# Kernel tuning notes

Measured on AMD Instinct MI355X. Metric: run time of the kernel, lower is better.

The kernel has to match this reference:

```python
import jax, jax.numpy as jnp
import numpy as np

UNITS = 1024
D_MODEL = 1024
H = 16
DK = 64
DV = 64
M = 128
B = 4
S = 1024


def setup_inputs() -> dict:
    key = jax.random.key(0)
    ks = jax.random.split(key, 12)
    s = 1.0 / np.sqrt(D_MODEL)
    inp = {
        "queries": jax.random.normal(ks[0], (B, S, D_MODEL), jnp.float32),
        "keys": jax.random.normal(ks[1], (B, S, D_MODEL), jnp.float32),
        "values": jax.random.normal(ks[2], (B, S, D_MODEL), jnp.float32),
        "Wq": jax.random.normal(ks[3], (D_MODEL, H * DK), jnp.float32) * s,
        "bq": jnp.zeros((H * DK,), jnp.float32),
        "Wk": jax.random.normal(ks[4], (D_MODEL, H * DK), jnp.float32) * s,
        "bk": jnp.zeros((H * DK,), jnp.float32),
        "Wv": jax.random.normal(ks[5], (D_MODEL, H * DV), jnp.float32) * s,
        "bv": jnp.zeros((H * DV,), jnp.float32),
        "Wo": jax.random.normal(ks[6], (H * DV, UNITS), jnp.float32) * (1.0 / np.sqrt(H * DV)),
        "bo": jnp.zeros((UNITS,), jnp.float32),
        "mk": jax.random.normal(ks[7], (1, M, H * DK), jnp.float32) * 0.1,
        "mv": jax.random.normal(ks[8], (1, M, H * DV), jnp.float32) * 0.1,
        "h": H,
    }
    return inp


def reference(queries, keys, values, Wq, bq, Wk, bk, Wv, bv, Wo, bo, mk, mv, h):
    Bq, Sq, _ = queries.shape
    m = mk.shape[1]
    dk = Wk.shape[1] // h
    dv = Wv.shape[1] // h
    scale_m = jnp.sqrt(jnp.asarray(m, queries.dtype))

    # Q projection: [B, h, Sq, dk]
    q = (queries @ Wq + bq).reshape(Bq, Sq, h, dk).transpose(0, 2, 1, 3)

    # K/V projections with m learned memory slots concatenated on the seq axis
    k_flat = jnp.concatenate(
        [keys @ Wk + bk, scale_m * jnp.broadcast_to(mk, (Bq, m, h * dk))], axis=1
    )  # [B, Sk+m, h*dk]
    v_flat = jnp.concatenate(
        [values @ Wv + bv, scale_m * jnp.broadcast_to(mv, (Bq, m, h * dv))], axis=1
    )  # [B, Sk+m, h*dv]
    Skm = k_flat.shape[1]
    k = k_flat.reshape(Bq, Skm, h, dk).transpose(0, 2, 1, 3)  # [B, h, Sk+m, dk]
    v = v_flat.reshape(Bq, Skm, h, dv).transpose(0, 2, 1, 3)  # [B, h, Sk+m, dv]

    # Scaled dot-product attention over sequence + memory slots
    scores = jnp.einsum("bhqd,bhkd->bhqk", q, k) / jnp.sqrt(jnp.asarray(dk, q.dtype))
    attn = jax.nn.softmax(scores, axis=-1)  # [B, h, Sq, Sk+m]
    out = jnp.einsum("bhqk,bhkd->bhqd", attn, v)  # [B, h, Sq, dv]
    out = out.transpose(0, 2, 1, 3).reshape(Bq, Sq, h * dv)
    return out @ Wo + bo
```

## Files before the change

### kernel.cpp

```cpp
#include <hip/hip_runtime.h>

typedef __attribute__((ext_vector_type(8))) __bf16 bf16x8;
typedef __attribute__((ext_vector_type(4))) float f32x4;

#define DEVINL __device__ __forceinline__

constexpr int BZ = 4;
constexpr int SEQ = 1024;
constexpr int DMODEL = 1024;
constexpr int NH = 16;
constexpr int HD = 64;
constexpr int MSLOT = 128;
constexpr int NT = BZ * SEQ;
constexpr int SKM = SEQ + MSLOT;
constexpr int VT_LD = BZ * SKM;
constexpr float SCALE_M = 11.313708498984761f;
constexpr float SCEXP = 0.18033688011112042f;
constexpr size_t OF_QIN  = 0;
constexpr size_t OF_KIN  = OF_QIN  + (size_t)NT * DMODEL;
constexpr size_t OF_VIN  = OF_KIN  + (size_t)NT * DMODEL;
constexpr size_t OF_WQT  = OF_VIN  + (size_t)NT * DMODEL;
constexpr size_t OF_WKT  = OF_WQT  + (size_t)DMODEL * DMODEL;
constexpr size_t OF_WVT  = OF_WKT  + (size_t)DMODEL * DMODEL;
constexpr size_t OF_WOT  = OF_WVT  + (size_t)DMODEL * DMODEL;
constexpr size_t OF_QB   = OF_WOT  + (size_t)DMODEL * DMODEL;
constexpr size_t OF_KPR  = OF_QB   + (size_t)NT * DMODEL;
constexpr size_t OF_KMEM = OF_KPR  + (size_t)NT * DMODEL;
constexpr size_t OF_VTG  = OF_KMEM + (size_t)MSLOT * DMODEL;
constexpr size_t OF_AOUT = OF_VTG  + (size_t)DMODEL * VT_LD;

DEVINL unsigned short f2bf(float f) {
  union { float f; unsigned u; } v; v.f = f;
  unsigned r = v.u + 0x7FFF + ((v.u >> 16) & 1);
  return (unsigned short)(r >> 16);
}

#if __has_builtin(__builtin_amdgcn_cvt_pk_bf16_f32)
DEVINL unsigned pack2(float a, float b) {
  auto t = __builtin_amdgcn_cvt_pk_bf16_f32(a, b);
  unsigned r; __builtin_memcpy(&r, &t, 4); return r;
}
#else
DEVINL unsigned pack2(float a, float b) {
  return (unsigned)f2bf(a) | ((unsigned)f2bf(b) << 16);
}
#endif

#if __has_builtin(__builtin_amdgcn_exp2f)
DEVINL float fast_exp2(float x) { return __builtin_amdgcn_exp2f(x); }
#else
DEVINL float fast_exp2(float x) { return exp2f(x); }
#endif

DEVINL f32x4 mfma16(bf16x8 a, bf16x8 b, f32x4 c) {
  return __builtin_amdgcn_mfma_f32_16x16x32_bf16(a, b, c, 0, 0, 0);
}

DEVINL void gload16(const unsigned short* gp, unsigned short* lp) {
  __builtin_amdgcn_global_load_lds(
      (const __attribute__((address_space(1))) unsigned int*)(const void*)gp,
      (__attribute__((address_space(3))) unsigned int*)(void*)lp, 16, 0, 0);
}

__global__ __launch_bounds__(256) void prep_all(
    const float* __restrict__ q, const float* __restrict__ k, const float* __restrict__ v,
    const float* __restrict__ W0, const float* __restrict__ W1,
    const float* __restrict__ W2, const float* __restrict__ W3,
    const float* __restrict__ mk, const float* __restrict__ mv,
    unsigned short* __restrict__ dq, unsigned short* __restrict__ dk,
    unsigned short* __restrict__ dv,
    unsigned short* __restrict__ d0, unsigned short* __restrict__ d1,
    unsigned short* __restrict__ d2, unsigned short* __restrict__ d3,
    unsigned short* __restrict__ Kmm, unsigned short* __restrict__ VtG) {
  __shared__ float t[32][65];
  const int tid = threadIdx.x;
  const int bid = blockIdx.x;
  if (bid < 6144) {
    const int tz = bid >> 11;
    const float* src = (tz == 0) ? q : (tz == 1) ? k : v;
    unsigned short* dst = (tz == 0) ? dq : (tz == 1) ? dk : dv;
    int i = ((bid & 2047) * 256 + tid) * 8;
    float4 v0 = *(const float4*)(src + i);
    float4 v1 = *(const float4*)(src + i + 4);
    union { unsigned u2[4]; uint4 v; } o;
    o.u2[0] = pack2(v0.x, v0.y); o.u2[1] = pack2(v0.z, v0.w);
    o.u2[2] = pack2(v1.x, v1.y); o.u2[3] = pack2(v1.z, v1.w);
    *(uint4*)(dst + i) = o.v;
  } else if (bid < 8192) {
    const int rel = bid - 6144;
    const int z = rel >> 9, rem = rel & 511;
    const float* src = (z == 0) ? W0 : (z == 1) ? W1 : (z == 2) ? W2 : W3;
    unsigned short* dst = (z == 0) ? d0 : (z == 1) ? d1 : (z == 2) ? d2 : d3;
    const int n0 = (rem & 31) * 32, k0 = (rem >> 5) * 64;
    {
      int c = tid & 31, rg = tid >> 5;
#pragma unroll
      for (int rr = 0; rr < 8; ++rr)
        t[c][rg * 8 + rr] = src[(size_t)(k0 + rg * 8 + rr) * DMODEL + n0 + c];
    }
    __syncthreads();
    {
      int n = tid >> 3, ck = tid & 7;
      union { unsigned short u[8]; uint4 v; } o;
#pragma unroll
      for (int j = 0; j < 8; ++j) o.u[j] = f2bf(t[n][ck * 8 + j]);
      *(uint4*)(dst + (size_t)(n0 + n) * DMODEL + k0 + ck * 8) = o.v;
    }
  } else if (bid < 8704) {
    int i = (bid - 8192) * 256 + tid;
    Kmm[i] = f2bf(mk[i] * SCALE_M);
  } else {
    const int rel = bid - 8704;
    const int j0 = (rel & 3) * 32, c0 = (rel >> 2) * 32;
    const int tx = tid & 31, ty = tid >> 5;
#pragma unroll
    for (int r = 0; r < 4; ++r)
      t[ty + r * 8][tx] = mv[(size_t)(j0 + ty + r * 8) * DMODEL + c0 + tx];
    __syncthreads();
#pragma unroll
    for (int r = 0; r < 4; ++r) {
      int c = c0 + ty + r * 8;
      unsigned short vv = f2bf(t[tx][ty + r * 8] * SCALE_M);
#pragma unroll
      for (int bb = 0; bb < BZ; ++bb)
        VtG[(size_t)c * VT_LD + bb * SKM + SEQ + j0 + tx] = vv;
    }
  }
}

__global__ __launch_bounds__(256, 3) void proj_qkv(
    const unsigned short* __restrict__ Qin, const unsigned short* __restrict__ Kin,
    const unsigned short* __restrict__ Vin, const unsigned short* __restrict__ Wqt,
    const unsigned short* __restrict__ Wkt, const unsigned short* __restrict__ Wvt,
    const float* __restrict__ bq, const float* __restrict__ bk,
    const float* __restrict__ bv, unsigned short* __restrict__ Qbp,
    unsigned short* __restrict__ Kprp, unsigned short* __restrict__ VtG) {
  __shared__ unsigned short As0[128 * 32], As1[128 * 32];
  __shared__ unsigned short Bs0[128 * 32], Bs1[128 * 32];
  const int tid = threadIdx.x;
  const int pid = blockIdx.x >> 8;
  const int idx = blockIdx.x & 255;
  const int w = tid >> 6, lane = tid & 63, quad = lane >> 4, l16 = lane & 15;
  const int wr = w >> 1, wc = w & 1;
  const int mt = idx & 31, nt = idx >> 5;
  f32x4 acc[4][4] = {};

  const unsigned short* Abase;
  const unsigned short* Bbase;
  if (pid == 0)      { Abase = Qin + (size_t)(mt * 128) * DMODEL; Bbase = Wqt + (size_t)(nt * 128) * DMODEL; }
  else if (pid == 1) { Abase = Kin + (size_t)(mt * 128) * DMODEL; Bbase = Wkt + (size_t)(nt * 128) * DMODEL; }
  else               { Abase = Wvt + (size_t)(nt * 128) * DMODEL; Bbase = Vin + (size_t)(mt * 128) * DMODEL; }

  const int srow = tid >> 2, sslot = tid & 3;
  for (int kt = 0; kt < 16; ++kt) {
    const int k0 = kt * 64;
#pragma unroll
    for (int hb = 0; hb < 2; ++hb) {
      unsigned short* al = hb ? As1 : As0;
      unsigned short* bl = hb ? Bs1 : Bs0;
#pragma unroll
      for (int gi = 0; gi < 2; ++gi) {
        int g = gi * 256 + tid;
        int row = g >> 2, slot = g & 3;
        gload16(Abase + (size_t)row * DMODEL + k0 + hb * 32 + slot * 8, al + g * 8);
        gload16(Bbase + (size_t)row * DMODEL + k0 + hb * 32 + slot * 8, bl + g * 8);
      }
    }
    __syncthreads();
#pragma unroll
    for (int hb = 0; hb < 2; ++hb) {
      const unsigned short* al = hb ? As1 : As0;
      const unsigned short* bl = hb ? Bs1 : Bs0;
      bf16x8 af[4], bfr[4];
#pragma unroll
      for (int rb = 0; rb < 4; ++rb)
        af[rb] = *(const bf16x8*)(al + (wr * 64 + rb * 16 + l16) * 32 + quad * 8);
#pragma unroll
      for (int cb = 0; cb < 4; ++cb)
        bfr[cb] = *(const bf16x8*)(bl + (wc * 64 + cb * 16 + l16) * 32 + quad * 8);
#pragma unroll
      for (int rb = 0; rb < 4; ++rb)
#pragma unroll
        for (int cb = 0; cb < 4; ++cb)
          acc[rb][cb] = mfma16(af[rb], bfr[cb], acc[rb][cb]);
    }
    __syncthreads();
  }

  if (pid < 2) {
    const float* bias   = pid ? bk : bq;
    unsigned short* out = pid ? Kprp : Qbp;
    const float osc     = pid ? 1.0f : SCEXP;
    const int m0 = mt * 128, n0 = nt * 128;
#pragma unroll
    for (int rb = 0; rb < 4; ++rb)
#pragma unroll
      for (int cb = 0; cb < 4; ++cb)
#pragma unroll
        for (int r = 0; r < 4; ++r) {
          int row = m0 + wr * 64 + rb * 16 + quad * 4 + r;
          int col = n0 + wc * 64 + cb * 16 + l16;
          out[(size_t)row * DMODEL + col] = f2bf((acc[rb][cb][r] + bias[col]) * osc);
        }
  } else {
    const int t0 = mt * 128, n0 = nt * 128;
#pragma unroll
    for (int rb = 0; rb < 4; ++rb)
#pragma unroll
      for (int cb = 0; cb < 4; ++cb)
#pragma unroll
        for (int r = 0; r < 4; ++r) {
          int n = n0 + wr * 64 + rb * 16 + quad * 4 + r;
          int tok = t0 + wc * 64 + cb * 16 + l16;
          int col = tok + (tok >> 10) * MSLOT;
          VtG[(size_t)n * VT_LD + col] = f2bf(acc[rb][cb][r] + bv[n]);
        }
  }
}

__global__ __launch_bounds__(256) void gemm_out(const unsigned short* __restrict__ A,
                                                const unsigned short* __restrict__ Wt,
                                                const float* __restrict__ bias,
                                                float* __restrict__ Cout) {
  __shared__ unsigned short A0[64 * 32], A1[64 * 32];
  __shared__ unsigned short B0[64 * 32], B1[64 * 32];
  const int tid = threadIdx.x;
  const int idx = blockIdx.x;
  const int m0 = (idx & 63) * 64, n0 = (idx >> 6) * 64;
  const int w = tid >> 6, lane = tid & 63, quad = lane >> 4, l16 = lane & 15;
  const int wr = w >> 1, wc = w & 1;
  f32x4 acc[2][2] = {};
  const unsigned short* rA = A + (size_t)m0 * DMODEL;
  const unsigned short* rB = Wt + (size_t)n0 * DMODEL;
  const int srow = tid >> 2, sslot = tid & 3;
  for (int kt = 0; kt < 16; ++kt) {
    const int k0 = kt * 64;
    gload16(rA + (size_t)srow * DMODEL + k0 + sslot * 8, A0 + tid * 8);
    gload16(rA + (size_t)srow * DMODEL + k0 + 32 + sslot * 8, A1 + tid * 8);
    gload16(rB + (size_t)srow * DMODEL + k0 + sslot * 8, B0 + tid * 8);
    gload16(rB + (size_t)srow * DMODEL + k0 + 32 + sslot * 8, B1 + tid * 8);
    __syncthreads();
#pragma unroll
    for (int hb = 0; hb < 2; ++hb) {
      const unsigned short* al = hb ? A1 : A0;
      const unsigned short* bl = hb ? B1 : B0;
      bf16x8 af[2], bfr[2];
#pragma unroll
      for (int rb = 0; rb < 2; ++rb)
        af[rb] = *(const bf16x8*)(al + (wr * 32 + rb * 16 + l16) * 32 + quad * 8);
#pragma unroll
      for (int cb = 0; cb < 2; ++cb)
        bfr[cb] = *(const bf16x8*)(bl + (wc * 32 + cb * 16 + l16) * 32 + quad * 8);
#pragma unroll
      for (int rb = 0; rb < 2; ++rb)
#pragma unroll
        for (int cb = 0; cb < 2; ++cb)
          acc[rb][cb] = mfma16(af[rb], bfr[cb], acc[rb][cb]);
    }
    __syncthreads();
  }
#pragma unroll
  for (int rb = 0; rb < 2; ++rb)
#pragma unroll
    for (int cb = 0; cb < 2; ++cb)
#pragma unroll
      for (int r = 0; r < 4; ++r) {
        int row = m0 + wr * 32 + rb * 16 + quad * 4 + r;
        int col = n0 + wc * 32 + cb * 16 + l16;
        Cout[(size_t)row * DMODEL + col] = acc[rb][cb][r] + bias[col];
      }
}

__global__ __launch_bounds__(256) void attn_kernel(const unsigned short* __restrict__ Qb,
                                                   const unsigned short* __restrict__ Kproj,
                                                   const unsigned short* __restrict__ Kmem,
                                                   const unsigned short* __restrict__ VtG,
                                                   unsigned short* __restrict__ Aout) {
  __shared__ unsigned short Ks[2][64 * 64];
  __shared__ unsigned short Vs[2][64 * 64];
  __shared__ unsigned short Pl[4 * 16 * 64];
  const int tid = threadIdx.x;
  const int bh = blockIdx.x & 63, qb = blockIdx.x >> 6;
  const int b = bh & 3, h = bh >> 2;
  const int w = tid >> 6, lane = tid & 63, quad = lane >> 4, l16 = lane & 15;
  const int token0 = b * SEQ + qb * 64 + w * 16;
  unsigned short* Pw = Pl + w * 16 * 64;
  const int lx = l16 & 7;

  const int ck0 = 2 * w, ck1 = 2 * w + 1;
  const int lrow = lane >> 3;
  const int lslot = (lane & 7) ^ lrow;
  const size_t ksrc0 = (size_t)(8 * ck0 + lrow) * DMODEL + lslot * 8;
  const size_t ksrc1 = (size_t)(8 * ck1 + lrow) * DMODEL + lslot * 8;
  const size_t vsrc0 = (size_t)(8 * ck0 + lrow) * VT_LD + lslot * 8;
  const size_t vsrc1 = (size_t)(8 * ck1 + lrow) * VT_LD + lslot * 8;
  const int ldst0 = ck0 * 512 + lane * 8;
  const int ldst1 = ck1 * 512 + lane * 8;

  auto kbase = [&](int tile) -> const unsigned short* {
    return (tile < 16) ? Kproj + (size_t)(b * SEQ + tile * 64) * DMODEL + h * HD
                       : Kmem + (size_t)((tile - 16) * 64) * DMODEL + h * HD;
  };
  auto vbase = [&](int tile) -> const unsigned short* {
    int c0 = (tile < 16) ? b * SKM + tile * 64 : b * SKM + SEQ + (tile - 16) * 64;
    return VtG + (size_t)(h * HD) * VT_LD + c0;
  };

  auto stage = [&](int buf, int tile) {
    const unsigned short* kp = kbase(tile);
    const unsigned short* vp = vbase(tile);
    gload16(kp + ksrc0, Ks[buf] + ldst0);
    gload16(kp + ksrc1, Ks[buf] + ldst1);
    gload16(vp + vsrc0, Vs[buf] + ldst0);
    gload16(vp + vsrc1, Vs[buf] + ldst1);
  };

  bf16x8 qf[2];
#pragma unroll
  for (int t = 0; t < 2; ++t)
    qf[t] = *(const bf16x8*)(Qb + (size_t)(token0 + l16) * DMODEL + h * HD + t * 32 + quad * 8);

  bf16x8 ones;
  {
    union { unsigned short u[8]; bf16x8 v; } one8;
#pragma unroll
    for (int i = 0; i < 8; ++i) one8.u[i] = 0x3F80;
    ones = one8.v;
  }

  f32x4 O[4] = {};
  f32x4 Lacc = {};

  stage(0, 0);
  __syncthreads();

  for (int tile = 0; tile < 18; ++tile) {
    const int cur = tile & 1;
    if (tile < 17) stage(cur ^ 1, tile + 1);

    f32x4 sc[4] = {};
    __builtin_amdgcn_s_setprio(1);
#pragma unroll
    for (int c = 0; c < 4; ++c)
#pragma unroll
      for (int t = 0; t < 2; ++t) {
        bf16x8 kb = *(const bf16x8*)(Ks[cur] + (c * 16 + l16) * 64 +
                                     ((t * 4 + quad) ^ lx) * 8);
        sc[c] = mfma16(kb, qf[t], sc[c]);
      }
    __builtin_amdgcn_s_setprio(0);

#pragma unroll
    for (int c = 0; c < 4; ++c) {
      float p0 = fast_exp2(sc[c][0]);
      float p1 = fast_exp2(sc[c][1]);
      float p2 = fast_exp2(sc[c][2]);
      float p3 = fast_exp2(sc[c][3]);
      union { unsigned u[2]; } pk;
      pk.u[0] = pack2(p0, p1);
      pk.u[1] = pack2(p2, p3);
      *(uint2*)(Pw + l16 * 64 + ((2 * c + (quad >> 1)) ^ lx) * 8 + (quad & 1) * 4) =
          *(uint2*)pk.u;
    }
    __builtin_amdgcn_wave_barrier();

    __builtin_amdgcn_s_setprio(1);
#pragma unroll
    for (int t2 = 0; t2 < 2; ++t2) {
      bf16x8 pa = *(const bf16x8*)(Pw + l16 * 64 + ((t2 * 4 + quad) ^ lx) * 8);
      Lacc = mfma16(pa, ones, Lacc);
#pragma unroll
      for (int c2 = 0; c2 < 4; ++c2) {
        bf16x8 vb = *(const bf16x8*)(Vs[cur] + (c2 * 16 + l16) * 64 +
                                     ((t2 * 4 + quad) ^ lx) * 8);
        O[c2] = mfma16(pa, vb, O[c2]);
      }
    }
    __builtin_amdgcn_s_setprio(0);

    __syncthreads();
  }

#pragma unroll
  for (int r = 0; r < 4; ++r) {
    float inv = 1.0f / Lacc[r];
#pragma unroll
    for (int c2 = 0; c2 < 4; ++c2)
      Aout[(size_t)(token0 + quad * 4 + r) * DMODEL + h * HD + c2 * 16 + l16] =
          f2bf(O[c2][r] * inv);
  }
}

extern "C" void kernel_launch(void* const* d_in, const int* in_sizes, int n_in,
                              void* d_out, int out_size, void* d_ws, size_t ws_size,
                              hipStream_t stream) {
  const float* queries = (const float*)d_in[0];
  const float* keys    = (const float*)d_in[1];
  const float* values  = (const float*)d_in[2];
  const float* Wq = (const float*)d_in[3];
  const float* bq = (const float*)d_in[4];
  const float* Wk = (const float*)d_in[5];
  const float* bk = (const float*)d_in[6];
  const float* Wv = (const float*)d_in[7];
  const float* bv = (const float*)d_in[8];
  const float* Wo = (const float*)d_in[9];
  const float* bo = (const float*)d_in[10];
  const float* mk = (const float*)d_in[11];
  const float* mv = (const float*)d_in[12];

  unsigned short* ws = (unsigned short*)d_ws;
  unsigned short* Qin  = ws + OF_QIN;
  unsigned short* Kin  = ws + OF_KIN;
  unsigned short* Vin  = ws + OF_VIN;
  unsigned short* Wqt  = ws + OF_WQT;
  unsigned short* Wkt  = ws + OF_WKT;
  unsigned short* Wvt  = ws + OF_WVT;
  unsigned short* Wot  = ws + OF_WOT;
  unsigned short* Qbp  = ws + OF_QB;
  unsigned short* Kprp = ws + OF_KPR;
  unsigned short* Kmm  = ws + OF_KMEM;
  unsigned short* VtGp = ws + OF_VTG;
  unsigned short* Aoutp = ws + OF_AOUT;

  prep_all<<<8832, 256, 0, stream>>>(queries, keys, values, Wq, Wk, Wv, Wo, mk, mv,
                                     Qin, Kin, Vin, Wqt, Wkt, Wvt, Wot, Kmm, VtGp);

  proj_qkv<<<768, 256, 0, stream>>>(Qin, Kin, Vin, Wqt, Wkt, Wvt, bq, bk, bv,
                                    Qbp, Kprp, VtGp);

  attn_kernel<<<1024, 256, 0, stream>>>(Qbp, Kprp, Kmm, VtGp, Aoutp);

  gemm_out<<<1024, 256, 0, stream>>>(Aoutp, Wot, bo, (float*)d_out);
}
```

Measured before the change: 209.2 us.

## Load V tiles directly into registers instead of staging through LDS

The attention kernel stops staging V tiles in shared memory. Each wave now loads its V fragments from global memory straight into registers, double-buffered across two register sets, while K stays double-buffered in LDS. The loop is unrolled by two so the register buffers alternate. This removes the LDS writes and reads for V and halves LDS usage, at the cost of more registers and of four redundant global V loads per block (one per wave), which may reduce occupancy.

```diff
diff --git a/kernel.cpp b/kernel.cpp
--- a/kernel.cpp
+++ b/kernel.cpp
@@ -277,7 +277,6 @@
                                                    const unsigned short* __restrict__ VtG,
                                                    unsigned short* __restrict__ Aout) {
   __shared__ unsigned short Ks[2][64 * 64];
-  __shared__ unsigned short Vs[2][64 * 64];
   __shared__ unsigned short Pl[4 * 16 * 64];
   const int tid = threadIdx.x;
   const int bh = blockIdx.x & 63, qb = blockIdx.x >> 6;
@@ -292,8 +291,6 @@
   const int lslot = (lane & 7) ^ lrow;
   const size_t ksrc0 = (size_t)(8 * ck0 + lrow) * DMODEL + lslot * 8;
   const size_t ksrc1 = (size_t)(8 * ck1 + lrow) * DMODEL + lslot * 8;
-  const size_t vsrc0 = (size_t)(8 * ck0 + lrow) * VT_LD + lslot * 8;
-  const size_t vsrc1 = (size_t)(8 * ck1 + lrow) * VT_LD + lslot * 8;
   const int ldst0 = ck0 * 512 + lane * 8;
   const int ldst1 = ck1 * 512 + lane * 8;
 
@@ -306,13 +303,19 @@
     return VtG + (size_t)(h * HD) * VT_LD + c0;
   };
 
-  auto stage = [&](int buf, int tile) {
+  auto stageK = [&](int buf, int tile) {
     const unsigned short* kp = kbase(tile);
-    const unsigned short* vp = vbase(tile);
     gload16(kp + ksrc0, Ks[buf] + ldst0);
     gload16(kp + ksrc1, Ks[buf] + ldst1);
-    gload16(vp + vsrc0, Vs[buf] + ldst0);
-    gload16(vp + vsrc1, Vs[buf] + ldst1);
+  };
+  auto vload = [&](bf16x8 (&vr)[2][4], int tile) {
+    const unsigned short* vp = vbase(tile);
+#pragma unroll
+    for (int t2 = 0; t2 < 2; ++t2)
+#pragma unroll
+      for (int c2 = 0; c2 < 4; ++c2)
+        vr[t2][c2] = *(const bf16x8*)(vp + (size_t)(c2 * 16 + l16) * VT_LD +
+                                      (t2 * 4 + quad) * 8);
   };
 
   bf16x8 qf[2];
@@ -331,20 +334,14 @@
   f32x4 O[4] = {};
   f32x4 Lacc = {};
 
-  stage(0, 0);
-  __syncthreads();
-
-  for (int tile = 0; tile < 18; ++tile) {
-    const int cur = tile & 1;
-    if (tile < 17) stage(cur ^ 1, tile + 1);
-
+  auto tilecomp = [&](const unsigned short* Kbuf, bf16x8 (&vr)[2][4]) {
     f32x4 sc[4] = {};
     __builtin_amdgcn_s_setprio(1);
 #pragma unroll
     for (int c = 0; c < 4; ++c)
 #pragma unroll
       for (int t = 0; t < 2; ++t) {
-        bf16x8 kb = *(const bf16x8*)(Ks[cur] + (c * 16 + l16) * 64 +
+        bf16x8 kb = *(const bf16x8*)(Kbuf + (c * 16 + l16) * 64 +
                                      ((t * 4 + quad) ^ lx) * 8);
         sc[c] = mfma16(kb, qf[t], sc[c]);
       }
@@ -370,14 +367,27 @@
       bf16x8 pa = *(const bf16x8*)(Pw + l16 * 64 + ((t2 * 4 + quad) ^ lx) * 8);
       Lacc = mfma16(pa, ones, Lacc);
 #pragma unroll
-      for (int c2 = 0; c2 < 4; ++c2) {
-        bf16x8 vb = *(const bf16x8*)(Vs[cur] + (c2 * 16 + l16) * 64 +
-                                     ((t2 * 4 + quad) ^ lx) * 8);
-        O[c2] = mfma16(pa, vb, O[c2]);
-      }
+      for (int c2 = 0; c2 < 4; ++c2)
+        O[c2] = mfma16(pa, vr[t2][c2], O[c2]);
     }
     __builtin_amdgcn_s_setprio(0);
-
+  };
+
+  bf16x8 vrA[2][4], vrB[2][4];
+  vload(vrA, 0);
+  stageK(0, 0);
+  __syncthreads();
+
+  for (int p = 0; p < 9; ++p) {
+    vload(vrB, 2 * p + 1);
+    stageK(1, 2 * p + 1);
+    tilecomp(Ks[0], vrA);
+    __syncthreads();
+    if (p < 8) {
+      vload(vrA, 2 * p + 2);
+      stageK(0, 2 * p + 2);
+    }
+    tilecomp(Ks[1], vrB);
     __syncthreads();
   }
 
```

Result: slower. 249.8 us (+19.4%).

## Process 32 query rows per wave in attention to reuse K/V fragments

Applied to the files above, without the earlier changes.

Each wave in the attention kernel now handles two 16-row query groups, so a block covers 128 queries and the grid halves to 512 blocks. Every K and V fragment read from shared memory feeds two MFMAs, which halves the K/V global traffic and LDS reads per query. The tile loop is also unrolled by two with fixed buffer indices. In exchange register pressure and the P scratch buffer double, and the halved grid may leave compute units less busy.

```diff
diff --git a/kernel.cpp b/kernel.cpp
--- a/kernel.cpp
+++ b/kernel.cpp
@@ -151,7 +151,6 @@
   else if (pid == 1) { Abase = Kin + (size_t)(mt * 128) * DMODEL; Bbase = Wkt + (size_t)(nt * 128) * DMODEL; }
   else               { Abase = Wvt + (size_t)(nt * 128) * DMODEL; Bbase = Vin + (size_t)(mt * 128) * DMODEL; }
 
-  const int srow = tid >> 2, sslot = tid & 3;
   for (int kt = 0; kt < 16; ++kt) {
     const int k0 = kt * 64;
 #pragma unroll
@@ -278,13 +277,13 @@
                                                    unsigned short* __restrict__ Aout) {
   __shared__ unsigned short Ks[2][64 * 64];
   __shared__ unsigned short Vs[2][64 * 64];
-  __shared__ unsigned short Pl[4 * 16 * 64];
+  __shared__ unsigned short Pl[4 * 2 * 16 * 64];
   const int tid = threadIdx.x;
   const int bh = blockIdx.x & 63, qb = blockIdx.x >> 6;
   const int b = bh & 3, h = bh >> 2;
   const int w = tid >> 6, lane = tid & 63, quad = lane >> 4, l16 = lane & 15;
-  const int token0 = b * SEQ + qb * 64 + w * 16;
-  unsigned short* Pw = Pl + w * 16 * 64;
+  const int token0 = b * SEQ + qb * 128 + w * 32;
+  unsigned short* Pw = Pl + w * 2048;
   const int lx = l16 & 7;
 
   const int ck0 = 2 * w, ck1 = 2 * w + 1;
@@ -315,10 +314,13 @@
     gload16(vp + vsrc1, Vs[buf] + ldst1);
   };
 
-  bf16x8 qf[2];
-#pragma unroll
-  for (int t = 0; t < 2; ++t)
-    qf[t] = *(const bf16x8*)(Qb + (size_t)(token0 + l16) * DMODEL + h * HD + t * 32 + quad * 8);
+  bf16x8 qf[2][2];
+#pragma unroll
+  for (int g = 0; g < 2; ++g)
+#pragma unroll
+    for (int t = 0; t < 2; ++t)
+      qf[g][t] = *(const bf16x8*)(Qb + (size_t)(token0 + g * 16 + l16) * DMODEL +
+                                  h * HD + t * 32 + quad * 8);
 
   bf16x8 ones;
   {
@@ -328,66 +330,82 @@
     ones = one8.v;
   }
 
-  f32x4 O[4] = {};
-  f32x4 Lacc = {};
+  f32x4 O0[4] = {}, O1[4] = {};
+  f32x4 Lacc0 = {}, Lacc1 = {};
+
+  auto tilecomp = [&](const unsigned short* Kbuf, const unsigned short* Vbuf) {
+    f32x4 sc0[4] = {}, sc1[4] = {};
+    __builtin_amdgcn_s_setprio(1);
+#pragma unroll
+    for (int c = 0; c < 4; ++c)
+#pragma unroll
+      for (int t = 0; t < 2; ++t) {
+        bf16x8 kb = *(const bf16x8*)(Kbuf + (c * 16 + l16) * 64 +
+                                     ((t * 4 + quad) ^ lx) * 8);
+        sc0[c] = mfma16(kb, qf[0][t], sc0[c]);
+        sc1[c] = mfma16(kb, qf[1][t], sc1[c]);
+      }
+    __builtin_amdgcn_s_setprio(0);
+
+#pragma unroll
+    for (int g = 0; g < 2; ++g) {
+#pragma unroll
+      for (int c = 0; c < 4; ++c) {
+        const f32x4& s = g ? sc1[c] : sc0[c];
+        float p0 = fast_exp2(s[0]);
+        float p1 = fast_exp2(s[1]);
+        float p2 = fast_exp2(s[2]);
+        float p3 = fast_exp2(s[3]);
+        union { unsigned u[2]; } pk;
+        pk.u[0] = pack2(p0, p1);
+        pk.u[1] = pack2(p2, p3);
+        *(uint2*)(Pw + g * 1024 + l16 * 64 +
+                  ((2 * c + (quad >> 1)) ^ lx) * 8 + (quad & 1) * 4) = *(uint2*)pk.u;
+      }
+    }
+    __builtin_amdgcn_wave_barrier();
+
+    __builtin_amdgcn_s_setprio(1);
+#pragma unroll
+    for (int t2 = 0; t2 < 2; ++t2) {
+      bf16x8 pa0 = *(const bf16x8*)(Pw + l16 * 64 + ((t2 * 4 + quad) ^ lx) * 8);
+      bf16x8 pa1 = *(const bf16x8*)(Pw + 1024 + l16 * 64 + ((t2 * 4 + quad) ^ lx) * 8);
+      Lacc0 = mfma16(pa0, ones, Lacc0);
+      Lacc1 = mfma16(pa1, ones, Lacc1);
+#pragma unroll
+      for (int c2 = 0; c2 < 4; ++c2) {
+        bf16x8 vb = *(const bf16x8*)(Vbuf + (c2 * 16 + l16) * 64 +
+                                     ((t2 * 4 + quad) ^ lx) * 8);
+        O0[c2] = mfma16(pa0, vb, O0[c2]);
+        O1[c2] = mfma16(pa1, vb, O1[c2]);
+      }
+    }
+    __builtin_amdgcn_s_setprio(0);
+  };
 
   stage(0, 0);
   __syncthreads();
 
-  for (int tile = 0; tile < 18; ++tile) {
-    const int cur = tile & 1;
-    if (tile < 17) stage(cur ^ 1, tile + 1);
-
-    f32x4 sc[4] = {};
-    __builtin_amdgcn_s_setprio(1);
-#pragma unroll
-    for (int c = 0; c < 4; ++c)
-#pragma unroll
-      for (int t = 0; t < 2; ++t) {
-        bf16x8 kb = *(const bf16x8*)(Ks[cur] + (c * 16 + l16) * 64 +
-                                     ((t * 4 + quad) ^ lx) * 8);
-        sc[c] = mfma16(kb, qf[t], sc[c]);
-      }
-    __builtin_amdgcn_s_setprio(0);
-
-#pragma unroll
-    for (int c = 0; c < 4; ++c) {
-      float p0 = fast_exp2(sc[c][0]);
-      float p1 = fast_exp2(sc[c][1]);
-      float p2 = fast_exp2(sc[c][2]);
-      float p3 = fast_exp2(sc[c][3]);
-      union { unsigned u[2]; } pk;
-      pk.u[0] = pack2(p0, p1);
-      pk.u[1] = pack2(p2, p3);
-      *(uint2*)(Pw + l16 * 64 + ((2 * c + (quad >> 1)) ^ lx) * 8 + (quad & 1) * 4) =
-          *(uint2*)pk.u;
-    }
-    __builtin_amdgcn_wave_barrier();
-
-    __builtin_amdgcn_s_setprio(1);
-#pragma unroll
-    for (int t2 = 0; t2 < 2; ++t2) {
-      bf16x8 pa = *(const bf16x8*)(Pw + l16 * 64 + ((t2 * 4 + quad) ^ lx) * 8);
-      Lacc = mfma16(pa, ones, Lacc);
-#pragma unroll
-      for (int c2 = 0; c2 < 4; ++c2) {
-        bf16x8 vb = *(const bf16x8*)(Vs[cur] + (c2 * 16 + l16) * 64 +
-                                     ((t2 * 4 + quad) ^ lx) * 8);
-        O[c2] = mfma16(pa, vb, O[c2]);
-      }
-    }
-    __builtin_amdgcn_s_setprio(0);
-
+  for (int p = 0; p < 9; ++p) {
+    stage(1, 2 * p + 1);
+    tilecomp(Ks[0], Vs[0]);
+    __syncthreads();
+    if (p < 8) stage(0, 2 * p + 2);
+    tilecomp(Ks[1], Vs[1]);
     __syncthreads();
   }
 
 #pragma unroll
   for (int r = 0; r < 4; ++r) {
-    float inv = 1.0f / Lacc[r];
-#pragma unroll
-    for (int c2 = 0; c2 < 4; ++c2)
+    float inv0 = 1.0f / Lacc0[r];
+    float inv1 = 1.0f / Lacc1[r];
+#pragma unroll
+    for (int c2 = 0; c2 < 4; ++c2) {
       Aout[(size_t)(token0 + quad * 4 + r) * DMODEL + h * HD + c2 * 16 + l16] =
-          f2bf(O[c2][r] * inv);
+          f2bf(O0[c2][r] * inv0);
+      Aout[(size_t)(token0 + 16 + quad * 4 + r) * DMODEL + h * HD + c2 * 16 + l16] =
+          f2bf(O1[c2][r] * inv1);
+    }
   }
 }
 
@@ -428,7 +446,7 @@
   proj_qkv<<<768, 256, 0, stream>>>(Qin, Kin, Vin, Wqt, Wkt, Wvt, bq, bk, bv,
                                     Qbp, Kprp, VtGp);
 
-  attn_kernel<<<1024, 256, 0, stream>>>(Qbp, Kprp, Kmm, VtGp, Aoutp);
+  attn_kernel<<<512, 256, 0, stream>>>(Qbp, Kprp, Kmm, VtGp, Aoutp);
 
   gemm_out<<<1024, 256, 0, stream>>>(Aoutp, Wot, bo, (float*)d_out);
 }
```

Measured after the change: 201.8 us. 1.04x faster.

## Keep softmax probabilities in registers via permuted K row staging

Applied to the files above, without the earlier changes.

K rows are staged into shared memory in a permuted order (sig_inv), so each lane's MFMA score outputs line up with the A-operand layout of the PV MFMA. The exponentiated scores are then packed straight into bf16 registers, and the LDS round trip through the P scratch buffer, along with its wave barrier, goes away. The tile loop is also unrolled by two so the double-buffer indices are constant. The permutation has to match the MFMA output layout exactly, or the sums pair probabilities with the wrong V rows.

```diff
diff --git a/kernel.cpp b/kernel.cpp
--- a/kernel.cpp
+++ b/kernel.cpp
@@ -151,7 +151,6 @@
   else if (pid == 1) { Abase = Kin + (size_t)(mt * 128) * DMODEL; Bbase = Wkt + (size_t)(nt * 128) * DMODEL; }
   else               { Abase = Wvt + (size_t)(nt * 128) * DMODEL; Bbase = Vin + (size_t)(mt * 128) * DMODEL; }
 
-  const int srow = tid >> 2, sslot = tid & 3;
   for (int kt = 0; kt < 16; ++kt) {
     const int k0 = kt * 64;
 #pragma unroll
@@ -278,22 +277,24 @@
                                                    unsigned short* __restrict__ Aout) {
   __shared__ unsigned short Ks[2][64 * 64];
   __shared__ unsigned short Vs[2][64 * 64];
-  __shared__ unsigned short Pl[4 * 16 * 64];
   const int tid = threadIdx.x;
   const int bh = blockIdx.x & 63, qb = blockIdx.x >> 6;
   const int b = bh & 3, h = bh >> 2;
   const int w = tid >> 6, lane = tid & 63, quad = lane >> 4, l16 = lane & 15;
   const int token0 = b * SEQ + qb * 64 + w * 16;
-  unsigned short* Pw = Pl + w * 16 * 64;
   const int lx = l16 & 7;
 
   const int ck0 = 2 * w, ck1 = 2 * w + 1;
   const int lrow = lane >> 3;
   const int lslot = (lane & 7) ^ lrow;
-  const size_t ksrc0 = (size_t)(8 * ck0 + lrow) * DMODEL + lslot * 8;
-  const size_t ksrc1 = (size_t)(8 * ck1 + lrow) * DMODEL + lslot * 8;
-  const size_t vsrc0 = (size_t)(8 * ck0 + lrow) * VT_LD + lslot * 8;
-  const size_t vsrc1 = (size_t)(8 * ck1 + lrow) * VT_LD + lslot * 8;
+  const int R0 = 8 * ck0 + lrow, R1 = 8 * ck1 + lrow;
+  auto sig_inv = [](int R) {
+    return (R & 0x20) | ((R & 0x0C) << 1) | ((R & 0x10) >> 2) | (R & 3);
+  };
+  const size_t ksrc0 = (size_t)sig_inv(R0) * DMODEL + lslot * 8;
+  const size_t ksrc1 = (size_t)sig_inv(R1) * DMODEL + lslot * 8;
+  const size_t vsrc0 = (size_t)R0 * VT_LD + lslot * 8;
+  const size_t vsrc1 = (size_t)R1 * VT_LD + lslot * 8;
   const int ldst0 = ck0 * 512 + lane * 8;
   const int ldst1 = ck1 * 512 + lane * 8;
 
@@ -331,53 +332,54 @@
   f32x4 O[4] = {};
   f32x4 Lacc = {};
 
-  stage(0, 0);
-  __syncthreads();
-
-  for (int tile = 0; tile < 18; ++tile) {
-    const int cur = tile & 1;
-    if (tile < 17) stage(cur ^ 1, tile + 1);
-
+  auto tilecomp = [&](const unsigned short* Kbuf, const unsigned short* Vbuf) {
     f32x4 sc[4] = {};
     __builtin_amdgcn_s_setprio(1);
 #pragma unroll
     for (int c = 0; c < 4; ++c)
 #pragma unroll
       for (int t = 0; t < 2; ++t) {
-        bf16x8 kb = *(const bf16x8*)(Ks[cur] + (c * 16 + l16) * 64 +
+        bf16x8 kb = *(const bf16x8*)(Kbuf + (c * 16 + l16) * 64 +
                                      ((t * 4 + quad) ^ lx) * 8);
         sc[c] = mfma16(kb, qf[t], sc[c]);
       }
     __builtin_amdgcn_s_setprio(0);
 
-#pragma unroll
-    for (int c = 0; c < 4; ++c) {
-      float p0 = fast_exp2(sc[c][0]);
-      float p1 = fast_exp2(sc[c][1]);
-      float p2 = fast_exp2(sc[c][2]);
-      float p3 = fast_exp2(sc[c][3]);
-      union { unsigned u[2]; } pk;
-      pk.u[0] = pack2(p0, p1);
-      pk.u[1] = pack2(p2, p3);
-      *(uint2*)(Pw + l16 * 64 + ((2 * c + (quad >> 1)) ^ lx) * 8 + (quad & 1) * 4) =
-          *(uint2*)pk.u;
-    }
-    __builtin_amdgcn_wave_barrier();
+    float e[4][4];
+#pragma unroll
+    for (int c = 0; c < 4; ++c)
+#pragma unroll
+      for (int r = 0; r < 4; ++r)
+        e[c][r] = fast_exp2(sc[c][r]);
 
     __builtin_amdgcn_s_setprio(1);
 #pragma unroll
     for (int t2 = 0; t2 < 2; ++t2) {
-      bf16x8 pa = *(const bf16x8*)(Pw + l16 * 64 + ((t2 * 4 + quad) ^ lx) * 8);
-      Lacc = mfma16(pa, ones, Lacc);
+      union { unsigned u[4]; bf16x8 v; } pa;
+      pa.u[0] = pack2(e[2 * t2][0],     e[2 * t2][1]);
+      pa.u[1] = pack2(e[2 * t2][2],     e[2 * t2][3]);
+      pa.u[2] = pack2(e[2 * t2 + 1][0], e[2 * t2 + 1][1]);
+      pa.u[3] = pack2(e[2 * t2 + 1][2], e[2 * t2 + 1][3]);
+      Lacc = mfma16(pa.v, ones, Lacc);
 #pragma unroll
       for (int c2 = 0; c2 < 4; ++c2) {
-        bf16x8 vb = *(const bf16x8*)(Vs[cur] + (c2 * 16 + l16) * 64 +
+        bf16x8 vb = *(const bf16x8*)(Vbuf + (c2 * 16 + l16) * 64 +
                                      ((t2 * 4 + quad) ^ lx) * 8);
-        O[c2] = mfma16(pa, vb, O[c2]);
+        O[c2] = mfma16(pa.v, vb, O[c2]);
       }
     }
     __builtin_amdgcn_s_setprio(0);
-
+  };
+
+  stage(0, 0);
+  __syncthreads();
+
+  for (int p = 0; p < 9; ++p) {
+    stage(1, 2 * p + 1);
+    tilecomp(Ks[0], Vs[0]);
+    __syncthreads();
+    if (p < 8) stage(0, 2 * p + 2);
+    tilecomp(Ks[1], Vs[1]);
     __syncthreads();
   }
 
```

After: 205.4 us. About the same (-1.8%).
